# Kernel optimization log

Measured on AMD Instinct MI355X. Metric: run time of the kernel, lower is better.

## Reference

```python
import jax, jax.numpy as jnp
import numpy as np

N, H, V, K = 2048, 1024, 50304, 16
C = V // K  # tokens per POS cluster


def setup_inputs() -> dict:
    key = jax.random.key(0)
    kx, ky, kw, kl = jax.random.split(key, 4)
    x = jax.random.normal(kx, (N, H), dtype=jnp.float32)
    y = jax.random.randint(ky, (N,), 0, V, dtype=jnp.int32)
    # consistent POS label: token y belongs to cluster y // C
    y_pos = (y // C).astype(jnp.int32)
    # pos2token[i] = token ids of cluster i (equal contiguous partition)
    pos2token = jnp.arange(V, dtype=jnp.int32).reshape(K, C)
    # token_in_pos_id[i][v] = within-cluster index of token v in cluster i
    token_in_pos_id = jnp.broadcast_to(jnp.arange(V, dtype=jnp.int32) % C, (K, V))
    cluster_w = jax.random.normal(kw, (H, K), dtype=jnp.float32) * 0.02
    logits = jax.random.normal(kl, (H, V), dtype=jnp.float32) * 0.02
    return {"x": x, "y": y, "y_pos": y_pos, "pos2token": pos2token,
            "token_in_pos_id": token_in_pos_id, "cluster_w": cluster_w, "logits": logits}


def reference(x, y, y_pos, pos2token, token_in_pos_id, cluster_w, logits):
    # cluster (POS) log-probs: [N, K]
    cluster_ll = jax.nn.log_softmax(x @ cluster_w, axis=1)
    # per-cluster weight slices gathered once: [H, K, C]
    W = logits[:, pos2token.reshape(-1)].reshape(H, K, C)
    # tail logits for every token against every cluster's token set: [N, K, C]
    tail_lp = jax.nn.log_softmax(jnp.einsum('nh,hkc->nkc', x, W), axis=-1)
    n = jnp.arange(y.shape[0])
    within = token_in_pos_id[y_pos, y]          # within-cluster target id
    nll = -cluster_ll[n, y_pos] - tail_lp[n, y_pos, within]
    return nll
```

## Files before the change

### kernel.cpp

```cpp
#include <hip/hip_runtime.h>
#include <hip/hip_bf16.h>

#define NROW 2048
#define HDIM 1024
#define VOC  50304
#define KCL  16
#define CDIM 3144

#define MT 128
#define NT 128
#define BK 32
#define PK 36

#define WS_SUMEXP 0
#define WS_COUNTS 2048
#define WS_PART   2064
#define WS_ZTGT   4112
#define WS_TCOL   6160
#define WS_ROWS   8208

typedef __attribute__((ext_vector_type(8))) short short8;
typedef __attribute__((ext_vector_type(4))) short short4v;
typedef __attribute__((ext_vector_type(4))) float f32x4;

__device__ __forceinline__ ushort2 f2bf2(float a, float b) {
    union { __hip_bfloat162 h; ushort2 u; } cv;
    cv.h = __float22bfloat162_rn(float2{a, b});
    return cv.u;
}

__global__ void scatter_kernel(const int* __restrict__ y,
                               const int* __restrict__ y_pos,
                               const int* __restrict__ tip,
                               int* ws_i) {
    int n = blockIdx.x * 256 + threadIdx.x;
    if (n >= NROW) return;
    int kn = y_pos[n];
    int slot = atomicAdd(&ws_i[WS_COUNTS + kn], 1);
    ws_i[WS_ROWS + kn * NROW + slot] = n;
    ws_i[WS_TCOL + n] = tip[kn * VOC + y[n]];
}

__global__ void cluster_kernel(const float* __restrict__ x,
                               const float* __restrict__ cw,
                               const int* __restrict__ y_pos,
                               float* ws_f) {
    int wave = threadIdx.x >> 6;
    int lane = threadIdx.x & 63;
    int n = blockIdx.x * 4 + wave;
    float acc[KCL];
#pragma unroll
    for (int k = 0; k < KCL; k++) acc[k] = 0.f;
#pragma unroll
    for (int j = 0; j < 16; j++) {
        int h = j * 64 + lane;
        float xv = x[(size_t)n * HDIM + h];
        const float4* cwr = (const float4*)(cw + (size_t)h * KCL);
#pragma unroll
        for (int q = 0; q < 4; q++) {
            float4 w = cwr[q];
            acc[q * 4 + 0] += xv * w.x;
            acc[q * 4 + 1] += xv * w.y;
            acc[q * 4 + 2] += xv * w.z;
            acc[q * 4 + 3] += xv * w.w;
        }
    }
#pragma unroll
    for (int off = 32; off >= 1; off >>= 1) {
#pragma unroll
        for (int k = 0; k < KCL; k++) acc[k] += __shfl_down(acc[k], off);
    }
    if (lane == 0) {
        int kn = y_pos[n];
        float m = acc[0];
#pragma unroll
        for (int k = 1; k < KCL; k++) m = fmaxf(m, acc[k]);
        float s = 0.f;
        float skn = 0.f;
#pragma unroll
        for (int k = 0; k < KCL; k++) {
            s += __expf(acc[k] - m);
            skn = (k == kn) ? acc[k] : skn;
        }
        ws_f[WS_PART + n] = (m + __logf(s)) - skn;
    }
}

__launch_bounds__(256, 2)
__global__ void tail_kernel(const float* __restrict__ x,
                            const float* __restrict__ logits,
                            const int* ws_i, float* ws_f) {
    __shared__ short As[MT * PK];
    __shared__ short Bs[NT * PK];
    __shared__ int   lrow[MT];
    __shared__ int   ltcol[MT];
    __shared__ float rowsum[MT];

    const int k  = blockIdx.y;
    const int ct = blockIdx.x;
    const int rt = blockIdx.z;
    const int Mk = ws_i[WS_COUNTS + k];
    if (rt * MT >= Mk) return;

    const int tid = threadIdx.x;
    if (tid < MT) {
        int r = rt * MT + tid;
        int rid = (r < Mk) ? ws_i[WS_ROWS + k * NROW + r] : -1;
        lrow[tid]  = rid;
        ltcol[tid] = (rid >= 0) ? ws_i[WS_TCOL + rid] : -1;
        rowsum[tid] = 0.f;
    }
    __syncthreads();

    const int ai = tid >> 1;
    const int ah = (tid & 1) * 16;
    const int aRow = lrow[ai];
    const int bn  = tid & 127;
    const int bk0 = (tid >> 7) * 16;
    const int clB = ct * NT + bn;
    const int gcol = k * CDIM + ((clB < CDIM) ? clB : (CDIM - 1));

    const int w    = tid >> 6;
    const int l    = tid & 63;
    const int wr   = (w >> 1) * 64;
    const int wc   = (w & 1) * 64;
    const int quad = l >> 4;
    const int lm   = l & 15;

    f32x4 acc[4][4];
#pragma unroll
    for (int mi = 0; mi < 4; mi++)
#pragma unroll
        for (int ni = 0; ni < 4; ni++) acc[mi][ni] = (f32x4)(0.f);

    union frag_u { short4v s4[2]; short8 s8; };
    union stage_u { ushort2 u2[8]; short4v s4[4]; };

    for (int h0 = 0; h0 < HDIM; h0 += BK) {
        {
            stage_u ta;
            if (aRow >= 0) {
                const float4* src = (const float4*)(x + (size_t)aRow * HDIM + h0 + ah);
#pragma unroll
                for (int q = 0; q < 4; q++) {
                    float4 v = src[q];
                    ta.u2[q * 2 + 0] = f2bf2(v.x, v.y);
                    ta.u2[q * 2 + 1] = f2bf2(v.z, v.w);
                }
            } else {
#pragma unroll
                for (int q = 0; q < 8; q++) ta.u2[q] = ushort2{0, 0};
            }
            short4v* dst = (short4v*)&As[ai * PK + ah];
#pragma unroll
            for (int q = 0; q < 4; q++) dst[q] = ta.s4[q];
        }
        {
            stage_u tb;
            const float* bp = logits + (size_t)(h0 + bk0) * VOC + gcol;
#pragma unroll
            for (int j = 0; j < 8; j++) {
                float v0 = bp[(size_t)(2 * j) * VOC];
                float v1 = bp[(size_t)(2 * j + 1) * VOC];
                tb.u2[j] = f2bf2(v0, v1);
            }
            short4v* dst = (short4v*)&Bs[bn * PK + bk0];
#pragma unroll
            for (int q = 0; q < 4; q++) dst[q] = tb.s4[q];
        }
        __syncthreads();

        short8 a[4], b[4];
#pragma unroll
        for (int mi = 0; mi < 4; mi++) {
            frag_u f;
            const short4v* p = (const short4v*)&As[(wr + mi * 16 + lm) * PK + quad * 8];
            f.s4[0] = p[0]; f.s4[1] = p[1];
            a[mi] = f.s8;
        }
#pragma unroll
        for (int ni = 0; ni < 4; ni++) {
            frag_u f;
            const short4v* p = (const short4v*)&Bs[(wc + ni * 16 + lm) * PK + quad * 8];
            f.s4[0] = p[0]; f.s4[1] = p[1];
            b[ni] = f.s8;
        }
#pragma unroll
        for (int mi = 0; mi < 4; mi++)
#pragma unroll
            for (int ni = 0; ni < 4; ni++)
                acc[mi][ni] = __builtin_amdgcn_mfma_f32_16x16x32_bf16(
                    a[mi], b[ni], acc[mi][ni], 0, 0, 0);
        __syncthreads();
    }

#pragma unroll
    for (int mi = 0; mi < 4; mi++) {
#pragma unroll
        for (int r = 0; r < 4; r++) {
            int row_local = wr + mi * 16 + quad * 4 + r;
            int rid = lrow[row_local];
            int tc  = ltcol[row_local];
            float s = 0.f;
#pragma unroll
            for (int ni = 0; ni < 4; ni++) {
                int cl = ct * NT + wc + ni * 16 + lm;
                float z = acc[mi][ni][r];
                if (rid >= 0 && cl < CDIM) {
                    s += __expf(z);
                    if (cl == tc) ws_f[WS_ZTGT + rid] = z;
                }
            }
            s += __shfl_xor(s, 1);
            s += __shfl_xor(s, 2);
            s += __shfl_xor(s, 4);
            s += __shfl_xor(s, 8);
            if (lm == 0 && rid >= 0) atomicAdd(&rowsum[row_local], s);
        }
    }
    __syncthreads();
    if (tid < MT) {
        int rid = lrow[tid];
        if (rid >= 0) atomicAdd(&ws_f[WS_SUMEXP + rid], rowsum[tid]);
    }
}

__global__ void finalize_kernel(const float* ws_f, float* __restrict__ out) {
    int n = blockIdx.x * 256 + threadIdx.x;
    if (n >= NROW) return;
    out[n] = ws_f[WS_PART + n] + __logf(ws_f[WS_SUMEXP + n]) - ws_f[WS_ZTGT + n];
}

extern "C" void kernel_launch(void* const* d_in, const int* in_sizes, int n_in,
                              void* d_out, int out_size, void* d_ws, size_t ws_size,
                              hipStream_t stream) {
    const float* x      = (const float*)d_in[0];
    const int*   y      = (const int*)d_in[1];
    const int*   y_pos  = (const int*)d_in[2];
    const int*   tip    = (const int*)d_in[4];
    const float* cw     = (const float*)d_in[5];
    const float* logits = (const float*)d_in[6];
    float* out  = (float*)d_out;
    float* ws_f = (float*)d_ws;
    int*   ws_i = (int*)d_ws;

    hipMemsetAsync(d_ws, 0, (size_t)(NROW + KCL) * 4, stream);

    scatter_kernel<<<NROW / 256, 256, 0, stream>>>(y, y_pos, tip, ws_i);
    cluster_kernel<<<NROW / 4, 256, 0, stream>>>(x, cw, y_pos, ws_f);

    dim3 grid((CDIM + NT - 1) / NT, KCL, NROW / MT);
    tail_kernel<<<grid, 256, 0, stream>>>(x, logits, ws_i, ws_f);

    finalize_kernel<<<NROW / 256, 256, 0, stream>>>(ws_f, out);
}
```

Measured before the change: 342.7 us.

## Pre-convert inputs to bf16, transpose logits, use direct-to-LDS loads with compact tile plan

```diff
diff --git a/kernel.cpp b/kernel.cpp
--- a/kernel.cpp
+++ b/kernel.cpp
@@ -1,5 +1,6 @@
 #include <hip/hip_runtime.h>
 #include <hip/hip_bf16.h>
+#include <stdint.h>
 
 #define NROW 2048
 #define HDIM 1024
@@ -7,10 +8,10 @@
 #define KCL  16
 #define CDIM 3144
 
-#define MT 128
+#define MT 64
 #define NT 128
 #define BK 32
-#define PK 36
+#define MAXTILES 48
 
 #define WS_SUMEXP 0
 #define WS_COUNTS 2048
@@ -18,15 +19,27 @@
 #define WS_ZTGT   4112
 #define WS_TCOL   6160
 #define WS_ROWS   8208
-
+#define WS_NTILE  40976
+#define WS_TILES  40977
+#define WS_XB     65536
+#define WS_BT     (65536 + 1048576)
+
+typedef unsigned short u16;
 typedef __attribute__((ext_vector_type(8))) short short8;
-typedef __attribute__((ext_vector_type(4))) short short4v;
 typedef __attribute__((ext_vector_type(4))) float f32x4;
+typedef __attribute__((ext_vector_type(4))) unsigned short ushort4v;
+typedef __attribute__((ext_vector_type(8))) unsigned short ushort8v;
 
 __device__ __forceinline__ ushort2 f2bf2(float a, float b) {
     union { __hip_bfloat162 h; ushort2 u; } cv;
     cv.h = __float22bfloat162_rn(float2{a, b});
     return cv.u;
+}
+
+__device__ __forceinline__ void gload16(const void* g, void* lds) {
+    __builtin_amdgcn_global_load_lds(
+        (__attribute__((address_space(1))) void*)(g),
+        (__attribute__((address_space(3))) void*)(lds), 16, 0, 0);
 }
 
 __global__ void scatter_kernel(const int* __restrict__ y,
@@ -41,6 +54,22 @@
     ws_i[WS_TCOL + n] = tip[kn * VOC + y[n]];
 }
 
+__global__ void plan_kernel(int* ws_i) {
+    if (threadIdx.x == 0) {
+        int t = 0;
+        for (int k = 0; k < KCL; k++) {
+            int mk = ws_i[WS_COUNTS + k];
+            int nt = (mk + MT - 1) / MT;
+            for (int r = 0; r < nt; r++) {
+                ws_i[WS_TILES + 2 * t]     = k;
+                ws_i[WS_TILES + 2 * t + 1] = r;
+                t++;
+            }
+        }
+        ws_i[WS_NTILE] = t;
+    }
+}
+
 __global__ void cluster_kernel(const float* __restrict__ x,
                                const float* __restrict__ cw,
                                const int* __restrict__ y_pos,
@@ -75,8 +104,7 @@
         float m = acc[0];
 #pragma unroll
         for (int k = 1; k < KCL; k++) m = fmaxf(m, acc[k]);
-        float s = 0.f;
-        float skn = 0.f;
+        float s = 0.f, skn = 0.f;
 #pragma unroll
         for (int k = 0; k < KCL; k++) {
             s += __expf(acc[k] - m);
@@ -86,109 +114,120 @@
     }
 }
 
-__launch_bounds__(256, 2)
-__global__ void tail_kernel(const float* __restrict__ x,
-                            const float* __restrict__ logits,
+__global__ void convx_kernel(const float* __restrict__ x, u16* __restrict__ xb) {
+    int t = blockIdx.x * 256 + threadIdx.x;
+    float4 f = ((const float4*)x)[t];
+    ushort2 a = f2bf2(f.x, f.y);
+    ushort2 b = f2bf2(f.z, f.w);
+    ushort4v v = {a.x, a.y, b.x, b.y};
+    *(ushort4v*)(xb + (size_t)t * 4) = v;
+}
+
+#define TV 128
+#define TH 128
+#define THP 136
+__global__ void transpose_kernel(const float* __restrict__ L, u16* __restrict__ Bt) {
+    __shared__ u16 Ls[TV * THP];
+    const int v0 = blockIdx.x * TV;
+    const int h0 = blockIdx.y * TH;
+    const int t  = threadIdx.x;
+    {
+        const int vi = (t & 31) * 4;
+        const int hi = t >> 5;
+#pragma unroll
+        for (int p = 0; p < 16; p++) {
+            int hh = p * 8 + hi;
+            float4 f = *(const float4*)(L + (size_t)(h0 + hh) * VOC + v0 + vi);
+            ushort2 u01 = f2bf2(f.x, f.y);
+            ushort2 u23 = f2bf2(f.z, f.w);
+            Ls[(vi + 0) * THP + hh] = u01.x;
+            Ls[(vi + 1) * THP + hh] = u01.y;
+            Ls[(vi + 2) * THP + hh] = u23.x;
+            Ls[(vi + 3) * THP + hh] = u23.y;
+        }
+    }
+    __syncthreads();
+    {
+        const int hi = (t & 15) * 8;
+        const int vi = t >> 4;
+#pragma unroll
+        for (int p = 0; p < 8; p++) {
+            int v = p * 16 + vi;
+            ushort8v val = *(const ushort8v*)&Ls[v * THP + hi];
+            *(ushort8v*)(Bt + (size_t)(v0 + v) * HDIM + h0 + hi) = val;
+        }
+    }
+}
+
+__launch_bounds__(256, 4)
+__global__ void tail_kernel(const u16* __restrict__ xb,
+                            const u16* __restrict__ Bt,
                             const int* ws_i, float* ws_f) {
-    __shared__ short As[MT * PK];
-    __shared__ short Bs[NT * PK];
+    __shared__ __align__(16) u16 As[MT * BK];
+    __shared__ __align__(16) u16 Bs[NT * BK];
     __shared__ int   lrow[MT];
     __shared__ int   ltcol[MT];
     __shared__ float rowsum[MT];
 
-    const int k  = blockIdx.y;
-    const int ct = blockIdx.x;
-    const int rt = blockIdx.z;
-    const int Mk = ws_i[WS_COUNTS + k];
-    if (rt * MT >= Mk) return;
+    const int ntile = ws_i[WS_NTILE];
+    if ((int)blockIdx.y >= ntile) return;
+    const int kcl = ws_i[WS_TILES + 2 * blockIdx.y];
+    const int rt  = ws_i[WS_TILES + 2 * blockIdx.y + 1];
+    const int ct  = blockIdx.x;
+    const int Mk  = ws_i[WS_COUNTS + kcl];
 
     const int tid = threadIdx.x;
     if (tid < MT) {
         int r = rt * MT + tid;
-        int rid = (r < Mk) ? ws_i[WS_ROWS + k * NROW + r] : -1;
+        int rid = (r < Mk) ? ws_i[WS_ROWS + kcl * NROW + r] : -1;
         lrow[tid]  = rid;
         ltcol[tid] = (rid >= 0) ? ws_i[WS_TCOL + rid] : -1;
         rowsum[tid] = 0.f;
     }
     __syncthreads();
 
-    const int ai = tid >> 1;
-    const int ah = (tid & 1) * 16;
-    const int aRow = lrow[ai];
-    const int bn  = tid & 127;
-    const int bk0 = (tid >> 7) * 16;
-    const int clB = ct * NT + bn;
-    const int gcol = k * CDIM + ((clB < CDIM) ? clB : (CDIM - 1));
-
     const int w    = tid >> 6;
     const int l    = tid & 63;
-    const int wr   = (w >> 1) * 64;
-    const int wc   = (w & 1) * 64;
     const int quad = l >> 4;
     const int lm   = l & 15;
 
-    f32x4 acc[4][4];
+    int arow = w * 16 + (l >> 2);
+    int rid_s = lrow[arow]; if (rid_s < 0) rid_s = 0;
+    const u16* agp = xb + (size_t)rid_s * HDIM + (l & 3) * 8;
+    u16* alds = (u16*)As + w * 512;
+    int c0 = w * 32 + (l >> 2);
+    int c1 = c0 + 16;
+    int g0 = ct * NT + c0; if (g0 >= CDIM) g0 = CDIM - 1;
+    int g1 = ct * NT + c1; if (g1 >= CDIM) g1 = CDIM - 1;
+    const u16* bgp0 = Bt + (size_t)(kcl * CDIM + g0) * HDIM + (l & 3) * 8;
+    const u16* bgp1 = Bt + (size_t)(kcl * CDIM + g1) * HDIM + (l & 3) * 8;
+    u16* blds0 = (u16*)Bs + w * 1024;
+    u16* blds1 = (u16*)Bs + w * 1024 + 512;
+
+    f32x4 acc[4][2];
 #pragma unroll
     for (int mi = 0; mi < 4; mi++)
 #pragma unroll
-        for (int ni = 0; ni < 4; ni++) acc[mi][ni] = (f32x4)(0.f);
-
-    union frag_u { short4v s4[2]; short8 s8; };
-    union stage_u { ushort2 u2[8]; short4v s4[4]; };
+        for (int ni = 0; ni < 2; ni++) acc[mi][ni] = (f32x4)(0.f);
 
     for (int h0 = 0; h0 < HDIM; h0 += BK) {
-        {
-            stage_u ta;
-            if (aRow >= 0) {
-                const float4* src = (const float4*)(x + (size_t)aRow * HDIM + h0 + ah);
-#pragma unroll
-                for (int q = 0; q < 4; q++) {
-                    float4 v = src[q];
-                    ta.u2[q * 2 + 0] = f2bf2(v.x, v.y);
-                    ta.u2[q * 2 + 1] = f2bf2(v.z, v.w);
-                }
-            } else {
-#pragma unroll
-                for (int q = 0; q < 8; q++) ta.u2[q] = ushort2{0, 0};
-            }
-            short4v* dst = (short4v*)&As[ai * PK + ah];
-#pragma unroll
-            for (int q = 0; q < 4; q++) dst[q] = ta.s4[q];
-        }
-        {
-            stage_u tb;
-            const float* bp = logits + (size_t)(h0 + bk0) * VOC + gcol;
-#pragma unroll
-            for (int j = 0; j < 8; j++) {
-                float v0 = bp[(size_t)(2 * j) * VOC];
-                float v1 = bp[(size_t)(2 * j + 1) * VOC];
-                tb.u2[j] = f2bf2(v0, v1);
-            }
-            short4v* dst = (short4v*)&Bs[bn * PK + bk0];
-#pragma unroll
-            for (int q = 0; q < 4; q++) dst[q] = tb.s4[q];
-        }
+        gload16(agp, alds);
+        gload16(bgp0, blds0);
+        gload16(bgp1, blds1);
+        agp += BK; bgp0 += BK; bgp1 += BK;
         __syncthreads();
 
-        short8 a[4], b[4];
-#pragma unroll
-        for (int mi = 0; mi < 4; mi++) {
-            frag_u f;
-            const short4v* p = (const short4v*)&As[(wr + mi * 16 + lm) * PK + quad * 8];
-            f.s4[0] = p[0]; f.s4[1] = p[1];
-            a[mi] = f.s8;
-        }
-#pragma unroll
-        for (int ni = 0; ni < 4; ni++) {
-            frag_u f;
-            const short4v* p = (const short4v*)&Bs[(wc + ni * 16 + lm) * PK + quad * 8];
-            f.s4[0] = p[0]; f.s4[1] = p[1];
-            b[ni] = f.s8;
-        }
+        short8 a[4], b[2];
 #pragma unroll
         for (int mi = 0; mi < 4; mi++)
-#pragma unroll
-            for (int ni = 0; ni < 4; ni++)
+            a[mi] = *(const short8*)&As[(mi * 16 + lm) * BK + quad * 8];
+#pragma unroll
+        for (int ni = 0; ni < 2; ni++)
+            b[ni] = *(const short8*)&Bs[(w * 32 + ni * 16 + lm) * BK + quad * 8];
+#pragma unroll
+        for (int mi = 0; mi < 4; mi++)
+#pragma unroll
+            for (int ni = 0; ni < 2; ni++)
                 acc[mi][ni] = __builtin_amdgcn_mfma_f32_16x16x32_bf16(
                     a[mi], b[ni], acc[mi][ni], 0, 0, 0);
         __syncthreads();
@@ -198,13 +237,13 @@
     for (int mi = 0; mi < 4; mi++) {
 #pragma unroll
         for (int r = 0; r < 4; r++) {
-            int row_local = wr + mi * 16 + quad * 4 + r;
+            int row_local = mi * 16 + quad * 4 + r;
             int rid = lrow[row_local];
             int tc  = ltcol[row_local];
             float s = 0.f;
 #pragma unroll
-            for (int ni = 0; ni < 4; ni++) {
-                int cl = ct * NT + wc + ni * 16 + lm;
+            for (int ni = 0; ni < 2; ni++) {
+                int cl = ct * NT + w * 32 + ni * 16 + lm;
                 float z = acc[mi][ni][r];
                 if (rid >= 0 && cl < CDIM) {
                     s += __expf(z);
@@ -243,14 +282,19 @@
     float* out  = (float*)d_out;
     float* ws_f = (float*)d_ws;
     int*   ws_i = (int*)d_ws;
+    u16*   xb   = (u16*)((float*)d_ws + WS_XB);
+    u16*   Bt   = (u16*)((float*)d_ws + WS_BT);
 
     hipMemsetAsync(d_ws, 0, (size_t)(NROW + KCL) * 4, stream);
 
     scatter_kernel<<<NROW / 256, 256, 0, stream>>>(y, y_pos, tip, ws_i);
+    plan_kernel<<<1, 64, 0, stream>>>(ws_i);
     cluster_kernel<<<NROW / 4, 256, 0, stream>>>(x, cw, y_pos, ws_f);
-
-    dim3 grid((CDIM + NT - 1) / NT, KCL, NROW / MT);
-    tail_kernel<<<grid, 256, 0, stream>>>(x, logits, ws_i, ws_f);
+    convx_kernel<<<NROW * HDIM / 4 / 256, 256, 0, stream>>>(x, xb);
+    transpose_kernel<<<dim3(VOC / TV, HDIM / TH), 256, 0, stream>>>(logits, Bt);
+
+    dim3 grid((CDIM + NT - 1) / NT, MAXTILES);
+    tail_kernel<<<grid, 256, 0, stream>>>(xb, Bt, ws_i, ws_f);
 
     finalize_kernel<<<NROW / 256, 256, 0, stream>>>(ws_f, out);
 }
```

Result: slower. 394.8 us (+15.2%).

## Compact tile scheduling, reshape tail tiles to 64x256, prefetch operands in registers

Applied to the files above, without the earlier changes.

```diff
diff --git a/kernel.cpp b/kernel.cpp
--- a/kernel.cpp
+++ b/kernel.cpp
@@ -1,5 +1,6 @@
 #include <hip/hip_runtime.h>
 #include <hip/hip_bf16.h>
+#include <stdint.h>
 
 #define NROW 2048
 #define HDIM 1024
@@ -7,10 +8,12 @@
 #define KCL  16
 #define CDIM 3144
 
-#define MT 128
-#define NT 128
+#define MT 64
+#define NT 256
 #define BK 32
 #define PK 36
+#define NCT 13
+#define MAXTILES 48
 
 #define WS_SUMEXP 0
 #define WS_COUNTS 2048
@@ -18,10 +21,14 @@
 #define WS_ZTGT   4112
 #define WS_TCOL   6160
 #define WS_ROWS   8208
-
+#define WS_NTILE  40976
+#define WS_TILES  40977
+
+typedef unsigned short u16;
 typedef __attribute__((ext_vector_type(8))) short short8;
 typedef __attribute__((ext_vector_type(4))) short short4v;
 typedef __attribute__((ext_vector_type(4))) float f32x4;
+typedef __attribute__((ext_vector_type(4))) unsigned short ushort4v;
 
 __device__ __forceinline__ ushort2 f2bf2(float a, float b) {
     union { __hip_bfloat162 h; ushort2 u; } cv;
@@ -41,6 +48,25 @@
     ws_i[WS_TCOL + n] = tip[kn * VOC + y[n]];
 }
 
+__global__ void plan_kernel(int* ws_i) {
+    int lane = threadIdx.x;
+    int nt = (lane < KCL) ? (ws_i[WS_COUNTS + lane] + MT - 1) / MT : 0;
+    int pre = nt;
+#pragma unroll
+    for (int off = 1; off < 16; off <<= 1) {
+        int v = __shfl_up(pre, off);
+        if ((lane & 15) >= off) pre += v;
+    }
+    int start = pre - nt;
+    if (lane < KCL) {
+        for (int r = 0; r < nt; r++) {
+            ws_i[WS_TILES + 2 * (start + r)]     = lane;
+            ws_i[WS_TILES + 2 * (start + r) + 1] = r;
+        }
+        if (lane == KCL - 1) ws_i[WS_NTILE] = start + nt;
+    }
+}
+
 __global__ void cluster_kernel(const float* __restrict__ x,
                                const float* __restrict__ cw,
                                const int* __restrict__ y_pos,
@@ -75,8 +101,7 @@
         float m = acc[0];
 #pragma unroll
         for (int k = 1; k < KCL; k++) m = fmaxf(m, acc[k]);
-        float s = 0.f;
-        float skn = 0.f;
+        float s = 0.f, skn = 0.f;
 #pragma unroll
         for (int k = 0; k < KCL; k++) {
             s += __expf(acc[k] - m);
@@ -86,104 +111,102 @@
     }
 }
 
-__launch_bounds__(256, 2)
+__launch_bounds__(256)
 __global__ void tail_kernel(const float* __restrict__ x,
                             const float* __restrict__ logits,
                             const int* ws_i, float* ws_f) {
-    __shared__ short As[MT * PK];
-    __shared__ short Bs[NT * PK];
+    __shared__ __align__(16) u16 As[MT * PK];
+    __shared__ __align__(16) u16 Bs[NT * PK];
     __shared__ int   lrow[MT];
     __shared__ int   ltcol[MT];
     __shared__ float rowsum[MT];
 
-    const int k  = blockIdx.y;
-    const int ct = blockIdx.x;
-    const int rt = blockIdx.z;
-    const int Mk = ws_i[WS_COUNTS + k];
-    if (rt * MT >= Mk) return;
+    const int ntile = ws_i[WS_NTILE];
+    if ((int)blockIdx.y >= ntile) return;
+    const int kcl = ws_i[WS_TILES + 2 * blockIdx.y];
+    const int rt  = ws_i[WS_TILES + 2 * blockIdx.y + 1];
+    const int ct  = blockIdx.x;
+    const int Mk  = ws_i[WS_COUNTS + kcl];
 
     const int tid = threadIdx.x;
     if (tid < MT) {
         int r = rt * MT + tid;
-        int rid = (r < Mk) ? ws_i[WS_ROWS + k * NROW + r] : -1;
+        int rid = (r < Mk) ? ws_i[WS_ROWS + kcl * NROW + r] : -1;
         lrow[tid]  = rid;
         ltcol[tid] = (rid >= 0) ? ws_i[WS_TCOL + rid] : -1;
         rowsum[tid] = 0.f;
     }
     __syncthreads();
 
-    const int ai = tid >> 1;
-    const int ah = (tid & 1) * 16;
-    const int aRow = lrow[ai];
-    const int bn  = tid & 127;
-    const int bk0 = (tid >> 7) * 16;
-    const int clB = ct * NT + bn;
-    const int gcol = k * CDIM + ((clB < CDIM) ? clB : (CDIM - 1));
-
     const int w    = tid >> 6;
     const int l    = tid & 63;
-    const int wr   = (w >> 1) * 64;
-    const int wc   = (w & 1) * 64;
     const int quad = l >> 4;
     const int lm   = l & 15;
 
+    const int arow = tid >> 2;
+    const int ak0  = (tid & 3) * 8;
+    int rid_s = lrow[arow]; if (rid_s < 0) rid_s = 0;
+    const float* ap = x + (size_t)rid_s * HDIM + ak0;
+    int gc = ct * NT + tid; if (gc >= CDIM) gc = CDIM - 1;
+    const float* bp = logits + (size_t)(kcl * CDIM + gc);
+
+    float ar[8];
+    float br[BK];
+#pragma unroll
+    for (int j = 0; j < 8; j++) ar[j] = ap[j];
+#pragma unroll
+    for (int k = 0; k < BK; k++) br[k] = bp[(size_t)k * VOC];
+    ap += BK;
+    bp += (size_t)BK * VOC;
+
     f32x4 acc[4][4];
 #pragma unroll
     for (int mi = 0; mi < 4; mi++)
 #pragma unroll
         for (int ni = 0; ni < 4; ni++) acc[mi][ni] = (f32x4)(0.f);
 
-    union frag_u { short4v s4[2]; short8 s8; };
-    union stage_u { ushort2 u2[8]; short4v s4[4]; };
+    union fr { short4v h[2]; short8 s; };
 
     for (int h0 = 0; h0 < HDIM; h0 += BK) {
-        {
-            stage_u ta;
-            if (aRow >= 0) {
-                const float4* src = (const float4*)(x + (size_t)aRow * HDIM + h0 + ah);
-#pragma unroll
-                for (int q = 0; q < 4; q++) {
-                    float4 v = src[q];
-                    ta.u2[q * 2 + 0] = f2bf2(v.x, v.y);
-                    ta.u2[q * 2 + 1] = f2bf2(v.z, v.w);
-                }
-            } else {
-#pragma unroll
-                for (int q = 0; q < 8; q++) ta.u2[q] = ushort2{0, 0};
-            }
-            short4v* dst = (short4v*)&As[ai * PK + ah];
-#pragma unroll
-            for (int q = 0; q < 4; q++) dst[q] = ta.s4[q];
-        }
-        {
-            stage_u tb;
-            const float* bp = logits + (size_t)(h0 + bk0) * VOC + gcol;
-#pragma unroll
-            for (int j = 0; j < 8; j++) {
-                float v0 = bp[(size_t)(2 * j) * VOC];
-                float v1 = bp[(size_t)(2 * j + 1) * VOC];
-                tb.u2[j] = f2bf2(v0, v1);
-            }
-            short4v* dst = (short4v*)&Bs[bn * PK + bk0];
-#pragma unroll
-            for (int q = 0; q < 4; q++) dst[q] = tb.s4[q];
+#pragma unroll
+        for (int jj = 0; jj < 2; jj++) {
+            ushort2 p0 = f2bf2(ar[jj * 4 + 0], ar[jj * 4 + 1]);
+            ushort2 p1 = f2bf2(ar[jj * 4 + 2], ar[jj * 4 + 3]);
+            ushort4v v = {p0.x, p0.y, p1.x, p1.y};
+            *(ushort4v*)&As[arow * PK + ak0 + jj * 4] = v;
+        }
+#pragma unroll
+        for (int j = 0; j < 8; j++) {
+            ushort2 p0 = f2bf2(br[j * 4 + 0], br[j * 4 + 1]);
+            ushort2 p1 = f2bf2(br[j * 4 + 2], br[j * 4 + 3]);
+            ushort4v v = {p0.x, p0.y, p1.x, p1.y};
+            *(ushort4v*)&Bs[tid * PK + j * 4] = v;
         }
         __syncthreads();
 
+        if (h0 + BK < HDIM) {
+#pragma unroll
+            for (int j = 0; j < 8; j++) ar[j] = ap[j];
+#pragma unroll
+            for (int k = 0; k < BK; k++) br[k] = bp[(size_t)k * VOC];
+            ap += BK;
+            bp += (size_t)BK * VOC;
+        }
+
         short8 a[4], b[4];
 #pragma unroll
         for (int mi = 0; mi < 4; mi++) {
-            frag_u f;
-            const short4v* p = (const short4v*)&As[(wr + mi * 16 + lm) * PK + quad * 8];
-            f.s4[0] = p[0]; f.s4[1] = p[1];
-            a[mi] = f.s8;
+            fr f;
+            const short4v* p = (const short4v*)&As[(mi * 16 + lm) * PK + quad * 8];
+            f.h[0] = p[0]; f.h[1] = p[1];
+            a[mi] = f.s;
         }
 #pragma unroll
         for (int ni = 0; ni < 4; ni++) {
-            frag_u f;
-            const short4v* p = (const short4v*)&Bs[(wc + ni * 16 + lm) * PK + quad * 8];
-            f.s4[0] = p[0]; f.s4[1] = p[1];
-            b[ni] = f.s8;
+            fr f;
+            const short4v* p = (const short4v*)&Bs[(w * 64 + ni * 16 + lm) * PK + quad * 8];
+            f.h[0] = p[0]; f.h[1] = p[1];
+            b[ni] = f.s;
         }
 #pragma unroll
         for (int mi = 0; mi < 4; mi++)
@@ -198,13 +221,13 @@
     for (int mi = 0; mi < 4; mi++) {
 #pragma unroll
         for (int r = 0; r < 4; r++) {
-            int row_local = wr + mi * 16 + quad * 4 + r;
+            int row_local = mi * 16 + quad * 4 + r;
             int rid = lrow[row_local];
             int tc  = ltcol[row_local];
             float s = 0.f;
 #pragma unroll
             for (int ni = 0; ni < 4; ni++) {
-                int cl = ct * NT + wc + ni * 16 + lm;
+                int cl = ct * NT + w * 64 + ni * 16 + lm;
                 float z = acc[mi][ni][r];
                 if (rid >= 0 && cl < CDIM) {
                     s += __expf(z);
@@ -247,9 +270,10 @@
     hipMemsetAsync(d_ws, 0, (size_t)(NROW + KCL) * 4, stream);
 
     scatter_kernel<<<NROW / 256, 256, 0, stream>>>(y, y_pos, tip, ws_i);
+    plan_kernel<<<1, 64, 0, stream>>>(ws_i);
     cluster_kernel<<<NROW / 4, 256, 0, stream>>>(x, cw, y_pos, ws_f);
 
-    dim3 grid((CDIM + NT - 1) / NT, KCL, NROW / MT);
+    dim3 grid(NCT, MAXTILES);
     tail_kernel<<<grid, 256, 0, stream>>>(x, logits, ws_i, ws_f);
 
     finalize_kernel<<<NROW / 256, 256, 0, stream>>>(ws_f, out);
```

Result: no change. 345.4 us (+0.8%).
